# Performance work log

Measured on AMD Instinct MI355X. Metric: run time of the kernel, lower is better.

## Reference

```python
import jax, jax.numpy as jnp
import numpy as np

Q = 10        # icosahedral diamonds
M = 128       # 2**dggrid_level
L = Q * M * M # 163840 icosahedral points
KS = 9        # kernel_size / knn neighbors


def setup_inputs() -> dict:
    key = jax.random.key(0)
    k1, k2, k3, k4 = jax.random.split(key, 4)
    b, c, h, w = 1, 128, 256, 512
    x = jax.random.normal(k1, (b, c, h, w), dtype=jnp.float32)
    codeskmin = jax.random.randint(k2, (L, KS), 0, h * w, dtype=jnp.int32)
    att_w = jax.random.normal(k3, (KS, 2, KS), dtype=jnp.float32) * 0.1
    att_b = jnp.zeros((KS,), dtype=jnp.float32)
    depth_w = jax.random.normal(k4, (c, KS), dtype=jnp.float32) * 0.1
    depth_b = jnp.zeros((c,), dtype=jnp.float32)
    gamma = jnp.ones((c,), dtype=jnp.float32)
    beta = jnp.zeros((c,), dtype=jnp.float32)
    return {"x": x, "codeskmin": codeskmin, "att_w": att_w, "att_b": att_b,
            "depth_w": depth_w, "depth_b": depth_b, "gamma": gamma, "beta": beta}


def reference(x, codeskmin, att_w, att_b, depth_w, depth_b, gamma, beta):
    b, c, h, w = x.shape
    xf = x.reshape(b, c, h * w)
    # KNN gather: (b, c, L, KS)
    xe = xf[:, :, codeskmin]
    # --- SpatialAttentionModule_v1 ---
    avg = jnp.mean(xe, axis=1)           # (b, L, KS)
    mx = jnp.max(xe, axis=1)             # (b, L, KS)
    feat = jnp.stack([avg, mx], axis=1)  # (b, 2, L, KS)
    # Conv2d(2 -> KS, kernel (1,KS), no pad): reduces neighbor axis fully
    att = jnp.einsum('bilk,oik->bol', feat, att_w) + att_b[None, :, None]  # (b, KS, L)
    att = jax.nn.sigmoid(att)
    att = att.transpose(0, 2, 1)[:, None, :, :]  # (b, 1, L, KS)
    xe = att * xe + xe
    # --- depthwise conv over neighbor axis ---
    out = jnp.einsum('bclk,ck->bcl', xe, depth_w) + depth_b[None, :, None]  # (b, c, L)
    # rearrange 'b c (q h w) -> (b q) c h w'
    out = out.reshape(b, c, Q, M, M).transpose(0, 2, 1, 3, 4).reshape(b * Q, c, M, M)
    # BatchNorm (training-mode batch stats)
    mean = jnp.mean(out, axis=(0, 2, 3), keepdims=True)
    var = jnp.var(out, axis=(0, 2, 3), keepdims=True)
    out = (out - mean) * jax.lax.rsqrt(var + 1e-5)
    out = out * gamma[None, :, None, None] + beta[None, :, None, None]
    # Swish
    out = out * jax.nn.sigmoid(out)
    return out
```

## Files before the change

### kernel.cpp

```cpp
#include <hip/hip_runtime.h>
#include <hip/hip_bf16.h>

#define HW 131072
#define NCH 128
#define KS 9
#define L_TOTAL 163840
#define LPW 16

typedef float        f32x2 __attribute__((ext_vector_type(2)));
typedef float        f32x4 __attribute__((ext_vector_type(4)));

static __device__ __forceinline__ float bflo(unsigned int p) { return __uint_as_float(p << 16); }
static __device__ __forceinline__ float bfhi(unsigned int p) { return __uint_as_float(p & 0xffff0000u); }
static __device__ __forceinline__ unsigned short f2bf(float f) {
    unsigned int x = __float_as_uint(f);
    return (unsigned short)((x + 0x7fffu + ((x >> 16) & 1u)) >> 16);
}
static __device__ __forceinline__ unsigned int pack2(float a, float b) {
    return (unsigned int)f2bf(a) | ((unsigned int)f2bf(b) << 16);
}

__global__ __launch_bounds__(256) void transpose_x_kernel(
    const f32x2* __restrict__ xf,
    unsigned int* __restrict__ xT,
    float2* __restrict__ meanmaxP)
{
    __shared__ unsigned short tile[128 * 128];
    __shared__ float ps[4][128];
    __shared__ float pm[4][128];
    const int tid = threadIdx.x;
    const int lane = tid & 63;
    const int wave = tid >> 6;
    const int p0 = blockIdx.x * 128;
    const int pa = 2 * lane, pb = 2 * lane + 1;

    float s0 = 0.f, s1 = 0.f;
    float m0 = -3.4e38f, m1 = -3.4e38f;
    #pragma unroll 8
    for (int it = 0; it < 32; ++it) {
        int c = wave + (it << 2);
        f32x2 v = __builtin_nontemporal_load(&xf[(long)c * (HW / 2) + (p0 >> 1) + lane]);
        tile[pa * 128 + ((c + 2 * pa) & 127)] = f2bf(v.x);
        tile[pb * 128 + ((c + 2 * pb) & 127)] = f2bf(v.y);
        s0 += v.x; s1 += v.y;
        m0 = fmaxf(m0, v.x); m1 = fmaxf(m1, v.y);
    }
    ps[wave][pa] = s0; ps[wave][pb] = s1;
    pm[wave][pa] = m0; pm[wave][pb] = m1;
    __syncthreads();

    #pragma unroll 8
    for (int it = 0; it < 32; ++it) {
        int p = wave + (it << 2);
        int colr = (2 * lane + 2 * p) & 127;
        unsigned int d = *reinterpret_cast<const unsigned int*>(&tile[p * 128 + colr]);
        xT[(long)(p0 + p) * 64 + lane] = d;
    }
    if (tid < 128) {
        float s = ps[0][tid] + ps[1][tid] + ps[2][tid] + ps[3][tid];
        float m = fmaxf(fmaxf(pm[0][tid], pm[1][tid]), fmaxf(pm[2][tid], pm[3][tid]));
        meanmaxP[p0 + tid] = make_float2(s * 0.0078125f, m);
    }
}

__global__ __launch_bounds__(256, 6) void encoder_main_kernel(
    const unsigned int* __restrict__ xT,
    const float2* __restrict__ meanmaxP,
    const int* __restrict__ cks,
    const float* __restrict__ att_w,
    const float* __restrict__ att_b,
    const float* __restrict__ depth_w,
    const float* __restrict__ depth_b,
    unsigned int* __restrict__ ybuf,
    float* __restrict__ gsum, float* __restrict__ gsq)
{
    __shared__ __align__(16) char smem[6080];
    float* attw   = (float*)smem;
    float* attb   = (float*)(smem + 648);
    int*   lcks   = (int*)(smem + 688);
    float* mult12 = (float*)(smem + 2992);
    float* red    = (float*)smem;

    const int tid = threadIdx.x;
    const int lane = tid & 63;
    const int wave = tid >> 6;
    const int c0 = lane * 2, c1 = c0 + 1;
    const int base_l = blockIdx.x * 64;

    if (tid < 162) attw[tid] = att_w[tid];
    if (tid < KS) attb[tid] = att_b[tid];
    for (int j = tid; j < 64 * KS; j += 256) lcks[j] = cks[base_l * KS + j];

    float dw0[KS], dw1[KS];
    #pragma unroll
    for (int k = 0; k < KS; ++k) {
        dw0[k] = depth_w[c0 * KS + k];
        dw1[k] = depth_w[c1 * KS + k];
    }
    const float db0 = depth_b[c0], db1 = depth_b[c1];
    __syncthreads();

    {
        const int l_local = tid >> 2;
        const int sub = tid & 3;
        if (sub < 3) {
            float mean[KS], mx[KS];
            #pragma unroll
            for (int k = 0; k < KS; ++k) {
                float2 mm = meanmaxP[lcks[l_local * KS + k]];
                mean[k] = mm.x; mx[k] = mm.y;
            }
            #pragma unroll
            for (int oo = 0; oo < 3; ++oo) {
                int o = sub * 3 + oo;
                float logit = attb[o];
                #pragma unroll
                for (int k = 0; k < KS; ++k) {
                    logit = fmaf(mean[k], attw[o * 18 + k], logit);
                    logit = fmaf(mx[k],   attw[o * 18 + 9 + k], logit);
                }
                mult12[l_local * 12 + o] = 1.0f + 1.0f / (1.0f + __expf(-logit));
            }
        }
    }
    __syncthreads();

    float sum0 = 0.f, sum1 = 0.f, sq0 = 0.f, sq1 = 0.f;
    const int lw0 = base_l + wave * LPW;

    #pragma unroll
    for (int li = 0; li < LPW; ++li) {
        const int l = __builtin_amdgcn_readfirstlane(lw0 + li);
        const int* ckp = cks + (long)l * KS;
        int idx[KS];
        #pragma unroll
        for (int k = 0; k < KS; ++k) idx[k] = ckp[k];

        unsigned int pv[KS];
        #pragma unroll
        for (int k = 0; k < KS; ++k) {
            const unsigned int* rowp = xT + ((long)idx[k] << 6);
            pv[k] = rowp[lane];
        }

        const int ll = wave * LPW + li;
        f32x4 mA = *(const f32x4*)&mult12[ll * 12 + 0];
        f32x4 mB = *(const f32x4*)&mult12[ll * 12 + 4];
        float m8 = mult12[ll * 12 + 8];
        float mk[KS] = {mA.x, mA.y, mA.z, mA.w, mB.x, mB.y, mB.z, mB.w, m8};

        float acc0 = db0, acc1 = db1;
        #pragma unroll
        for (int k = 0; k < KS; ++k) {
            acc0 = fmaf(bflo(pv[k]) * mk[k], dw0[k], acc0);
            acc1 = fmaf(bfhi(pv[k]) * mk[k], dw1[k], acc1);
        }

        ybuf[(long)l * 64 + lane] = pack2(acc0, acc1);
        sum0 += acc0; sum1 += acc1;
        sq0 = fmaf(acc0, acc0, sq0);
        sq1 = fmaf(acc1, acc1, sq1);
    }

    __syncthreads();
    red[0 * 256 + tid] = sum0;
    red[1 * 256 + tid] = sum1;
    red[2 * 256 + tid] = sq0;
    red[3 * 256 + tid] = sq1;
    __syncthreads();

    const int grp = tid >> 6;
    const int i = tid & 63;
    float t = red[grp * 256 + i] + red[grp * 256 + 64 + i] +
              red[grp * 256 + 128 + i] + red[grp * 256 + 192 + i];
    float* dst = (grp & 2) ? gsq : gsum;
    atomicAdd(&dst[2 * i + (grp & 1)], t);
}

__global__ __launch_bounds__(256) void finalize_kernel(
    const unsigned int* __restrict__ ybuf,
    const float* __restrict__ gsum, const float* __restrict__ gsq,
    const float* __restrict__ gamma, const float* __restrict__ beta,
    float* __restrict__ out)
{
    __shared__ unsigned short tile[128 * 130];
    const int tid = threadIdx.x;
    const int lane = tid & 63;
    const int wave = tid >> 6;
    const int q = blockIdx.x >> 7;
    const int r0 = (blockIdx.x & 127) * 128;
    const int c0 = 2 * lane, c1 = c0 + 1;

    const long lbase = (long)q * 16384 + r0;
    #pragma unroll 8
    for (int it = 0; it < 32; ++it) {
        int r = wave + (it << 2);
        unsigned int u = __builtin_nontemporal_load(&ybuf[(lbase + r) * 64 + lane]);
        tile[c0 * 130 + r] = (unsigned short)(u & 0xffffu);
        tile[c1 * 130 + r] = (unsigned short)(u >> 16);
    }
    __syncthreads();

    const float invN = 1.0f / (float)L_TOTAL;
    #pragma unroll 4
    for (int it = 0; it < 32; ++it) {
        int c = wave + (it << 2);
        float m = gsum[c] * invN;
        float var = gsq[c] * invN - m * m;
        float sc = gamma[c] * rsqrtf(var + 1e-5f);
        float sh = beta[c] - m * sc;
        unsigned int d = *reinterpret_cast<const unsigned int*>(&tile[c * 130 + 2 * lane]);
        float z0 = fmaf(bflo(d), sc, sh);
        float z1 = fmaf(bfhi(d), sc, sh);
        f32x2 v;
        v.x = z0 / (1.0f + __expf(-z0));
        v.y = z1 / (1.0f + __expf(-z1));
        *(f32x2*)&out[((long)(q * NCH + c) << 14) + r0 + 2 * lane] = v;
    }
}

extern "C" void kernel_launch(void* const* d_in, const int* in_sizes, int n_in,
                              void* d_out, int out_size, void* d_ws, size_t ws_size,
                              hipStream_t stream) {
    const f32x2* x_f2  = (const f32x2*)d_in[0];
    const int* cks     = (const int*)d_in[1];
    const float* aw    = (const float*)d_in[2];
    const float* ab    = (const float*)d_in[3];
    const float* dw    = (const float*)d_in[4];
    const float* db    = (const float*)d_in[5];
    const float* gm    = (const float*)d_in[6];
    const float* bt    = (const float*)d_in[7];

    char* ws = (char*)d_ws;
    unsigned int* xT   = (unsigned int*)ws;
    float2* meanmaxP   = (float2*)(ws + 33554432);
    unsigned int* ybuf = (unsigned int*)(ws + 34603008);
    float* gsum        = (float*)(ws + 34603008 + 41943040);
    float* gsq         = gsum + NCH;

    hipMemsetAsync(gsum, 0, 2 * NCH * sizeof(float), stream);

    transpose_x_kernel<<<HW / 128, 256, 0, stream>>>(x_f2, xT, meanmaxP);
    encoder_main_kernel<<<L_TOTAL / 64, 256, 0, stream>>>(
        xT, meanmaxP, cks, aw, ab, dw, db, ybuf, gsum, gsq);
    finalize_kernel<<<1280, 256, 0, stream>>>(
        ybuf, gsum, gsq, gm, bt, (float*)d_out);
}
```

Before: 316.9 us.

## Software-pipeline neighbor gathers three rows ahead using LDS-staged indices

The main kernel now reads neighbor indices from a padded LDS copy (stride 12) instead of global memory, and keeps gathers for the next three points in flight in a rotating register buffer. The first three gathers are issued before the barrier, overlapping them with the attention computation. Stores to ybuf become nontemporal, the index load is nontemporal, and occupancy is lowered from 6 to 5 waves per SIMD to make room for the extra registers. This trades occupancy for more memory-level parallelism per wave on the random-gather loop.

```diff
diff --git a/kernel.cpp b/kernel.cpp
--- a/kernel.cpp
+++ b/kernel.cpp
@@ -63,7 +63,19 @@
     }
 }
 
-__global__ __launch_bounds__(256, 6) void encoder_main_kernel(
+#define GLD(IDX) (*(const unsigned int*)(xTc + (((unsigned)(IDX)) << 8) + (unsigned)lane4))
+#define ISSUE9(B, A0, A1, A8)            \
+    pv[B][0] = GLD((A0).x);              \
+    pv[B][1] = GLD((A0).y);              \
+    pv[B][2] = GLD((A0).z);              \
+    pv[B][3] = GLD((A0).w);              \
+    pv[B][4] = GLD((A1).x);              \
+    pv[B][5] = GLD((A1).y);              \
+    pv[B][6] = GLD((A1).z);              \
+    pv[B][7] = GLD((A1).w);              \
+    pv[B][8] = GLD(A8)
+
+__global__ __launch_bounds__(256, 5) void encoder_main_kernel(
     const unsigned int* __restrict__ xT,
     const float2* __restrict__ meanmaxP,
     const int* __restrict__ cks,
@@ -74,11 +86,11 @@
     unsigned int* __restrict__ ybuf,
     float* __restrict__ gsum, float* __restrict__ gsq)
 {
-    __shared__ __align__(16) char smem[6080];
+    __shared__ __align__(16) char smem[6832];
     float* attw   = (float*)smem;
     float* attb   = (float*)(smem + 648);
     int*   lcks   = (int*)(smem + 688);
-    float* mult12 = (float*)(smem + 2992);
+    float* mult12 = (float*)(smem + 3760);
     float* red    = (float*)smem;
 
     const int tid = threadIdx.x;
@@ -86,10 +98,15 @@
     const int wave = tid >> 6;
     const int c0 = lane * 2, c1 = c0 + 1;
     const int base_l = blockIdx.x * 64;
+    const int lane4 = lane << 2;
+    const char* xTc = (const char*)xT;
 
     if (tid < 162) attw[tid] = att_w[tid];
     if (tid < KS) attb[tid] = att_b[tid];
-    for (int j = tid; j < 64 * KS; j += 256) lcks[j] = cks[base_l * KS + j];
+    for (int j = tid; j < 64 * KS; j += 256) {
+        const int lj = j / KS;
+        lcks[lj * 12 + (j - lj * KS)] = __builtin_nontemporal_load(&cks[base_l * KS + j]);
+    }
 
     float dw0[KS], dw1[KS];
     #pragma unroll
@@ -107,7 +124,7 @@
             float mean[KS], mx[KS];
             #pragma unroll
             for (int k = 0; k < KS; ++k) {
-                float2 mm = meanmaxP[lcks[l_local * KS + k]];
+                float2 mm = meanmaxP[lcks[l_local * 12 + k]];
                 mean[k] = mm.x; mx[k] = mm.y;
             }
             #pragma unroll
@@ -123,43 +140,68 @@
             }
         }
     }
+
+    const int ll0 = wave * LPW;
+    unsigned int pv[3][KS];
+
+    #pragma unroll
+    for (int li = 0; li < 3; ++li) {
+        const int p = (ll0 + li) * 12;
+        const int4 i0 = *(const int4*)&lcks[p];
+        const int4 i1 = *(const int4*)&lcks[p + 4];
+        const int  i8 = lcks[p + 8];
+        ISSUE9(li, i0, i1, i8);
+    }
+
     __syncthreads();
 
     float sum0 = 0.f, sum1 = 0.f, sq0 = 0.f, sq1 = 0.f;
-    const int lw0 = base_l + wave * LPW;
 
     #pragma unroll
     for (int li = 0; li < LPW; ++li) {
-        const int l = __builtin_amdgcn_readfirstlane(lw0 + li);
-        const int* ckp = cks + (long)l * KS;
-        int idx[KS];
-        #pragma unroll
-        for (int k = 0; k < KS; ++k) idx[k] = ckp[k];
-
-        unsigned int pv[KS];
-        #pragma unroll
-        for (int k = 0; k < KS; ++k) {
-            const unsigned int* rowp = xT + ((long)idx[k] << 6);
-            pv[k] = rowp[lane];
+        int4 ni0 = make_int4(0, 0, 0, 0), ni1 = make_int4(0, 0, 0, 0);
+        int ni8 = 0;
+        if (li + 3 < LPW) {
+            const int p = (ll0 + li + 3) * 12;
+            ni0 = *(const int4*)&lcks[p];
+            ni1 = *(const int4*)&lcks[p + 4];
+            ni8 = lcks[p + 8];
         }
 
-        const int ll = wave * LPW + li;
-        f32x4 mA = *(const f32x4*)&mult12[ll * 12 + 0];
-        f32x4 mB = *(const f32x4*)&mult12[ll * 12 + 4];
-        float m8 = mult12[ll * 12 + 8];
-        float mk[KS] = {mA.x, mA.y, mA.z, mA.w, mB.x, mB.y, mB.z, mB.w, m8};
-
+        const int ll = ll0 + li;
+        const f32x4 mA = *(const f32x4*)&mult12[ll * 12 + 0];
+        const f32x4 mB = *(const f32x4*)&mult12[ll * 12 + 4];
+        const float m8 = mult12[ll * 12 + 8];
         float acc0 = db0, acc1 = db1;
-        #pragma unroll
-        for (int k = 0; k < KS; ++k) {
-            acc0 = fmaf(bflo(pv[k]) * mk[k], dw0[k], acc0);
-            acc1 = fmaf(bfhi(pv[k]) * mk[k], dw1[k], acc1);
-        }
-
-        ybuf[(long)l * 64 + lane] = pack2(acc0, acc1);
+
+        acc0 = fmaf(bflo(pv[li % 3][0]) * mA.x, dw0[0], acc0);
+        acc1 = fmaf(bfhi(pv[li % 3][0]) * mA.x, dw1[0], acc1);
+        acc0 = fmaf(bflo(pv[li % 3][1]) * mA.y, dw0[1], acc0);
+        acc1 = fmaf(bfhi(pv[li % 3][1]) * mA.y, dw1[1], acc1);
+        acc0 = fmaf(bflo(pv[li % 3][2]) * mA.z, dw0[2], acc0);
+        acc1 = fmaf(bfhi(pv[li % 3][2]) * mA.z, dw1[2], acc1);
+        acc0 = fmaf(bflo(pv[li % 3][3]) * mA.w, dw0[3], acc0);
+        acc1 = fmaf(bfhi(pv[li % 3][3]) * mA.w, dw1[3], acc1);
+        acc0 = fmaf(bflo(pv[li % 3][4]) * mB.x, dw0[4], acc0);
+        acc1 = fmaf(bfhi(pv[li % 3][4]) * mB.x, dw1[4], acc1);
+        acc0 = fmaf(bflo(pv[li % 3][5]) * mB.y, dw0[5], acc0);
+        acc1 = fmaf(bfhi(pv[li % 3][5]) * mB.y, dw1[5], acc1);
+        acc0 = fmaf(bflo(pv[li % 3][6]) * mB.z, dw0[6], acc0);
+        acc1 = fmaf(bfhi(pv[li % 3][6]) * mB.z, dw1[6], acc1);
+        acc0 = fmaf(bflo(pv[li % 3][7]) * mB.w, dw0[7], acc0);
+        acc1 = fmaf(bfhi(pv[li % 3][7]) * mB.w, dw1[7], acc1);
+        acc0 = fmaf(bflo(pv[li % 3][8]) * m8,   dw0[8], acc0);
+        acc1 = fmaf(bfhi(pv[li % 3][8]) * m8,   dw1[8], acc1);
+
+        __builtin_nontemporal_store(pack2(acc0, acc1),
+                                    &ybuf[(long)(base_l + ll) * 64 + lane]);
         sum0 += acc0; sum1 += acc1;
         sq0 = fmaf(acc0, acc0, sq0);
         sq1 = fmaf(acc1, acc1, sq1);
+
+        if (li + 3 < LPW) {
+            ISSUE9(li % 3, ni0, ni1, ni8);
+        }
     }
 
     __syncthreads();
```

Result: slower. 347.2 us (+9.5%).

## Split channels into 8 slabs for gather and move attention logits to separate kernel

Applied to the files above, without the earlier changes.

Lays out the bf16 transposed input and the intermediate output as 8 channel-group slabs of 16 channels each. The gather kernel now has each block handle one channel group, with 8 lanes per point, so each neighbor fetch reads 32 bytes from a smaller, more cache-resident slab instead of a 256-byte row. The attention multipliers are computed in a new kernel and staged in global memory. This adds an extra launch and an extra buffer round-trip, and it reads the neighbor indices once per channel group.

```diff
diff --git a/kernel.cpp b/kernel.cpp
--- a/kernel.cpp
+++ b/kernel.cpp
@@ -5,7 +5,8 @@
 #define NCH 128
 #define KS 9
 #define L_TOTAL 163840
-#define LPW 16
+#define NGRP 8
+#define LPB 128
 
 typedef float        f32x2 __attribute__((ext_vector_type(2)));
 typedef float        f32x4 __attribute__((ext_vector_type(4)));
@@ -54,7 +55,7 @@
         int p = wave + (it << 2);
         int colr = (2 * lane + 2 * p) & 127;
         unsigned int d = *reinterpret_cast<const unsigned int*>(&tile[p * 128 + colr]);
-        xT[(long)(p0 + p) * 64 + lane] = d;
+        xT[((long)(lane >> 3) * HW + (p0 + p)) * 8 + (lane & 7)] = d;
     }
     if (tid < 128) {
         float s = ps[0][tid] + ps[1][tid] + ps[2][tid] + ps[3][tid];
@@ -63,34 +64,80 @@
     }
 }
 
-__global__ __launch_bounds__(256, 6) void encoder_main_kernel(
-    const unsigned int* __restrict__ xT,
+__global__ __launch_bounds__(256) void mult_kernel(
     const float2* __restrict__ meanmaxP,
     const int* __restrict__ cks,
     const float* __restrict__ att_w,
     const float* __restrict__ att_b,
+    float* __restrict__ multg)
+{
+    __shared__ float attw[162];
+    __shared__ float attb[12];
+    __shared__ int lcks[64 * 12];
+    const int tid = threadIdx.x;
+    const int base_l = blockIdx.x * 64;
+
+    if (tid < 162) attw[tid] = att_w[tid];
+    if (tid < KS) attb[tid] = att_b[tid];
+    for (int j = tid; j < 64 * KS; j += 256) {
+        const int lj = j / KS;
+        lcks[lj * 12 + (j - lj * KS)] = cks[(long)base_l * KS + j];
+    }
+    __syncthreads();
+
+    const int l_local = tid >> 2;
+    const int sub = tid & 3;
+    if (sub < 3) {
+        float mean[KS], mx[KS];
+        #pragma unroll
+        for (int k = 0; k < KS; ++k) {
+            float2 mm = meanmaxP[lcks[l_local * 12 + k]];
+            mean[k] = mm.x; mx[k] = mm.y;
+        }
+        #pragma unroll
+        for (int oo = 0; oo < 3; ++oo) {
+            int o = sub * 3 + oo;
+            float logit = attb[o];
+            #pragma unroll
+            for (int k = 0; k < KS; ++k) {
+                logit = fmaf(mean[k], attw[o * 18 + k], logit);
+                logit = fmaf(mx[k],   attw[o * 18 + 9 + k], logit);
+            }
+            multg[(long)(base_l + l_local) * 12 + o] = 1.0f + 1.0f / (1.0f + __expf(-logit));
+        }
+    }
+}
+
+__global__ __launch_bounds__(256, 6) void gather_kernel(
+    const unsigned int* __restrict__ xT,
+    const int* __restrict__ cks,
+    const float* __restrict__ multg,
     const float* __restrict__ depth_w,
     const float* __restrict__ depth_b,
     unsigned int* __restrict__ ybuf,
     float* __restrict__ gsum, float* __restrict__ gsq)
 {
-    __shared__ __align__(16) char smem[6080];
-    float* attw   = (float*)smem;
-    float* attb   = (float*)(smem + 648);
-    int*   lcks   = (int*)(smem + 688);
-    float* mult12 = (float*)(smem + 2992);
-    float* red    = (float*)smem;
-
-    const int tid = threadIdx.x;
+    __shared__ __align__(16) char smem[12288];
+    int*   lcks = (int*)smem;
+    float* mult = (float*)(smem + 6144);
+    float* red  = (float*)smem;
+
+    const int tid  = threadIdx.x;
     const int lane = tid & 63;
     const int wave = tid >> 6;
-    const int c0 = lane * 2, c1 = c0 + 1;
-    const int base_l = blockIdx.x * 64;
-
-    if (tid < 162) attw[tid] = att_w[tid];
-    if (tid < KS) attb[tid] = att_b[tid];
-    for (int j = tid; j < 64 * KS; j += 256) lcks[j] = cks[base_l * KS + j];
-
+    const int g      = blockIdx.x & 7;
+    const int base_l = (blockIdx.x >> 3) * LPB;
+    const int d    = lane & 7;
+    const int lsub = lane >> 3;
+
+    for (int j = tid; j < LPB * KS; j += 256) {
+        const int lj = j / KS;
+        lcks[lj * 12 + (j - lj * KS)] = __builtin_nontemporal_load(&cks[(long)base_l * KS + j]);
+    }
+    for (int j = tid; j < LPB * 12; j += 256)
+        mult[j] = __builtin_nontemporal_load(&multg[(long)base_l * 12 + j]);
+
+    const int c0 = g * 16 + 2 * d, c1 = c0 + 1;
     float dw0[KS], dw1[KS];
     #pragma unroll
     for (int k = 0; k < KS; ++k) {
@@ -98,65 +145,56 @@
         dw1[k] = depth_w[c1 * KS + k];
     }
     const float db0 = depth_b[c0], db1 = depth_b[c1];
-    __syncthreads();
-
-    {
-        const int l_local = tid >> 2;
-        const int sub = tid & 3;
-        if (sub < 3) {
-            float mean[KS], mx[KS];
-            #pragma unroll
-            for (int k = 0; k < KS; ++k) {
-                float2 mm = meanmaxP[lcks[l_local * KS + k]];
-                mean[k] = mm.x; mx[k] = mm.y;
-            }
-            #pragma unroll
-            for (int oo = 0; oo < 3; ++oo) {
-                int o = sub * 3 + oo;
-                float logit = attb[o];
-                #pragma unroll
-                for (int k = 0; k < KS; ++k) {
-                    logit = fmaf(mean[k], attw[o * 18 + k], logit);
-                    logit = fmaf(mx[k],   attw[o * 18 + 9 + k], logit);
-                }
-                mult12[l_local * 12 + o] = 1.0f + 1.0f / (1.0f + __expf(-logit));
-            }
-        }
-    }
+
+    const unsigned int* slab  = xT   + (long)g * HW * 8;
+    unsigned int*       yslab = ybuf + (long)g * L_TOTAL * 8;
     __syncthreads();
 
     float sum0 = 0.f, sum1 = 0.f, sq0 = 0.f, sq1 = 0.f;
-    const int lw0 = base_l + wave * LPW;
+    const int l0 = wave * (LPB / 4);
 
     #pragma unroll
-    for (int li = 0; li < LPW; ++li) {
-        const int l = __builtin_amdgcn_readfirstlane(lw0 + li);
-        const int* ckp = cks + (long)l * KS;
-        int idx[KS];
-        #pragma unroll
-        for (int k = 0; k < KS; ++k) idx[k] = ckp[k];
-
-        unsigned int pv[KS];
-        #pragma unroll
-        for (int k = 0; k < KS; ++k) {
-            const unsigned int* rowp = xT + ((long)idx[k] << 6);
-            pv[k] = rowp[lane];
-        }
-
-        const int ll = wave * LPW + li;
-        f32x4 mA = *(const f32x4*)&mult12[ll * 12 + 0];
-        f32x4 mB = *(const f32x4*)&mult12[ll * 12 + 4];
-        float m8 = mult12[ll * 12 + 8];
-        float mk[KS] = {mA.x, mA.y, mA.z, mA.w, mB.x, mB.y, mB.z, mB.w, m8};
+    for (int oct = 0; oct < LPB / 32; ++oct) {
+        const int l = l0 + oct * 8 + lsub;
+        const int4 i0 = *(const int4*)&lcks[l * 12];
+        const int4 i1 = *(const int4*)&lcks[l * 12 + 4];
+        const int  i8 = lcks[l * 12 + 8];
+
+        unsigned int pv0 = slab[(long)(unsigned)i0.x * 8 + d];
+        unsigned int pv1 = slab[(long)(unsigned)i0.y * 8 + d];
+        unsigned int pv2 = slab[(long)(unsigned)i0.z * 8 + d];
+        unsigned int pv3 = slab[(long)(unsigned)i0.w * 8 + d];
+        unsigned int pv4 = slab[(long)(unsigned)i1.x * 8 + d];
+        unsigned int pv5 = slab[(long)(unsigned)i1.y * 8 + d];
+        unsigned int pv6 = slab[(long)(unsigned)i1.z * 8 + d];
+        unsigned int pv7 = slab[(long)(unsigned)i1.w * 8 + d];
+        unsigned int pv8 = slab[(long)(unsigned)i8   * 8 + d];
+
+        const f32x4 mA = *(const f32x4*)&mult[l * 12];
+        const f32x4 mB = *(const f32x4*)&mult[l * 12 + 4];
+        const float m8 = mult[l * 12 + 8];
 
         float acc0 = db0, acc1 = db1;
-        #pragma unroll
-        for (int k = 0; k < KS; ++k) {
-            acc0 = fmaf(bflo(pv[k]) * mk[k], dw0[k], acc0);
-            acc1 = fmaf(bfhi(pv[k]) * mk[k], dw1[k], acc1);
-        }
-
-        ybuf[(long)l * 64 + lane] = pack2(acc0, acc1);
+        acc0 = fmaf(bflo(pv0) * mA.x, dw0[0], acc0);
+        acc1 = fmaf(bfhi(pv0) * mA.x, dw1[0], acc1);
+        acc0 = fmaf(bflo(pv1) * mA.y, dw0[1], acc0);
+        acc1 = fmaf(bfhi(pv1) * mA.y, dw1[1], acc1);
+        acc0 = fmaf(bflo(pv2) * mA.z, dw0[2], acc0);
+        acc1 = fmaf(bfhi(pv2) * mA.z, dw1[2], acc1);
+        acc0 = fmaf(bflo(pv3) * mA.w, dw0[3], acc0);
+        acc1 = fmaf(bfhi(pv3) * mA.w, dw1[3], acc1);
+        acc0 = fmaf(bflo(pv4) * mB.x, dw0[4], acc0);
+        acc1 = fmaf(bfhi(pv4) * mB.x, dw1[4], acc1);
+        acc0 = fmaf(bflo(pv5) * mB.y, dw0[5], acc0);
+        acc1 = fmaf(bfhi(pv5) * mB.y, dw1[5], acc1);
+        acc0 = fmaf(bflo(pv6) * mB.z, dw0[6], acc0);
+        acc1 = fmaf(bfhi(pv6) * mB.z, dw1[6], acc1);
+        acc0 = fmaf(bflo(pv7) * mB.w, dw0[7], acc0);
+        acc1 = fmaf(bfhi(pv7) * mB.w, dw1[7], acc1);
+        acc0 = fmaf(bflo(pv8) * m8,   dw0[8], acc0);
+        acc1 = fmaf(bfhi(pv8) * m8,   dw1[8], acc1);
+
+        yslab[(long)(base_l + l) * 8 + d] = pack2(acc0, acc1);
         sum0 += acc0; sum1 += acc1;
         sq0 = fmaf(acc0, acc0, sq0);
         sq1 = fmaf(acc1, acc1, sq1);
@@ -173,8 +211,18 @@
     const int i = tid & 63;
     float t = red[grp * 256 + i] + red[grp * 256 + 64 + i] +
               red[grp * 256 + 128 + i] + red[grp * 256 + 192 + i];
-    float* dst = (grp & 2) ? gsq : gsum;
-    atomicAdd(&dst[2 * i + (grp & 1)], t);
+    float* red2 = red + 1024;
+    red2[grp * 64 + i] = t;
+    __syncthreads();
+
+    if (tid < 32) {
+        const int q = tid >> 3, dd = tid & 7;
+        float s = 0.f;
+        #pragma unroll
+        for (int j = 0; j < 8; ++j) s += red2[q * 64 + j * 8 + dd];
+        float* dst = (q & 2) ? gsq : gsum;
+        atomicAdd(&dst[g * 16 + 2 * dd + (q & 1)], s);
+    }
 }
 
 __global__ __launch_bounds__(256) void finalize_kernel(
@@ -189,13 +237,15 @@
     const int wave = tid >> 6;
     const int q = blockIdx.x >> 7;
     const int r0 = (blockIdx.x & 127) * 128;
-    const int c0 = 2 * lane, c1 = c0 + 1;
+    const int gg = lane >> 3, dd = lane & 7;
+    const int c0 = gg * 16 + 2 * dd, c1 = c0 + 1;
 
     const long lbase = (long)q * 16384 + r0;
     #pragma unroll 8
     for (int it = 0; it < 32; ++it) {
         int r = wave + (it << 2);
-        unsigned int u = __builtin_nontemporal_load(&ybuf[(lbase + r) * 64 + lane]);
+        unsigned int u = __builtin_nontemporal_load(
+            &ybuf[((long)gg * L_TOTAL + lbase + r) * 8 + dd]);
         tile[c0 * 130 + r] = (unsigned short)(u & 0xffffu);
         tile[c1 * 130 + r] = (unsigned short)(u >> 16);
     }
@@ -235,14 +285,16 @@
     unsigned int* xT   = (unsigned int*)ws;
     float2* meanmaxP   = (float2*)(ws + 33554432);
     unsigned int* ybuf = (unsigned int*)(ws + 34603008);
-    float* gsum        = (float*)(ws + 34603008 + 41943040);
+    float* multg       = (float*)(ws + 76546048);
+    float* gsum        = (float*)(ws + 84410368);
     float* gsq         = gsum + NCH;
 
     hipMemsetAsync(gsum, 0, 2 * NCH * sizeof(float), stream);
 
     transpose_x_kernel<<<HW / 128, 256, 0, stream>>>(x_f2, xT, meanmaxP);
-    encoder_main_kernel<<<L_TOTAL / 64, 256, 0, stream>>>(
-        xT, meanmaxP, cks, aw, ab, dw, db, ybuf, gsum, gsq);
+    mult_kernel<<<L_TOTAL / 64, 256, 0, stream>>>(meanmaxP, cks, aw, ab, multg);
+    gather_kernel<<<(L_TOTAL / LPB) * NGRP, 256, 0, stream>>>(
+        xT, cks, multg, dw, db, ybuf, gsum, gsq);
     finalize_kernel<<<1280, 256, 0, stream>>>(
         ybuf, gsum, gsq, gm, bt, (float*)d_out);
 }
```

Result: faster. 303.4 us (-4.3%).

## Split channel-grouped gather into separate kernel with packed index/attention records

Applied to the files above, without the earlier changes.

Re-lays xT and ybuf into 8 channel-group slabs of 16 channels each, so each gather block touches a 4 MB slab that can stay L2-resident instead of scattering across the full 32 MB table. The attention multiplier is computed in a separate kernel and packed with the neighbor index into one 32-bit record (17-bit index, 15-bit quantized sigmoid). The gather kernel then reads these records and does 8-byte channel loads per lane, with shuffle-based stats reduction. This adds a kernel launch and quantizes the attention weight to 15 bits, which introduces small approximation error.

```diff
diff --git a/kernel.cpp b/kernel.cpp
--- a/kernel.cpp
+++ b/kernel.cpp
@@ -5,10 +5,13 @@
 #define NCH 128
 #define KS 9
 #define L_TOTAL 163840
-#define LPW 16
+#define NGRP 8
+#define LPB 128
 
 typedef float        f32x2 __attribute__((ext_vector_type(2)));
 typedef float        f32x4 __attribute__((ext_vector_type(4)));
+typedef unsigned int u32x2 __attribute__((ext_vector_type(2)));
+typedef unsigned int u32x4 __attribute__((ext_vector_type(4)));
 
 static __device__ __forceinline__ float bflo(unsigned int p) { return __uint_as_float(p << 16); }
 static __device__ __forceinline__ float bfhi(unsigned int p) { return __uint_as_float(p & 0xffff0000u); }
@@ -54,7 +57,7 @@
         int p = wave + (it << 2);
         int colr = (2 * lane + 2 * p) & 127;
         unsigned int d = *reinterpret_cast<const unsigned int*>(&tile[p * 128 + colr]);
-        xT[(long)(p0 + p) * 64 + lane] = d;
+        xT[((long)(lane >> 3) * HW + (p0 + p)) * 8 + (lane & 7)] = d;
     }
     if (tid < 128) {
         float s = ps[0][tid] + ps[1][tid] + ps[2][tid] + ps[3][tid];
@@ -63,118 +66,160 @@
     }
 }
 
-__global__ __launch_bounds__(256, 6) void encoder_main_kernel(
-    const unsigned int* __restrict__ xT,
+__global__ __launch_bounds__(256) void mult_kernel(
     const float2* __restrict__ meanmaxP,
     const int* __restrict__ cks,
     const float* __restrict__ att_w,
     const float* __restrict__ att_b,
+    unsigned int* __restrict__ rec)
+{
+    __shared__ float attw[162];
+    __shared__ float attb[12];
+    __shared__ int lcks[64 * 12];
+    const int tid = threadIdx.x;
+    const int base_l = blockIdx.x * 64;
+
+    if (tid < 162) attw[tid] = att_w[tid];
+    if (tid < KS) attb[tid] = att_b[tid];
+    for (int j = tid; j < 64 * KS; j += 256) {
+        const int lj = j / KS;
+        lcks[lj * 12 + (j - lj * KS)] = cks[(long)base_l * KS + j];
+    }
+    __syncthreads();
+
+    const int l_local = tid >> 2;
+    const int sub = tid & 3;
+    if (sub < 3) {
+        float mean[KS], mx[KS];
+        #pragma unroll
+        for (int k = 0; k < KS; ++k) {
+            float2 mm = meanmaxP[lcks[l_local * 12 + k]];
+            mean[k] = mm.x; mx[k] = mm.y;
+        }
+        #pragma unroll
+        for (int oo = 0; oo < 3; ++oo) {
+            int o = sub * 3 + oo;
+            float logit = attb[o];
+            #pragma unroll
+            for (int k = 0; k < KS; ++k) {
+                logit = fmaf(mean[k], attw[o * 18 + k], logit);
+                logit = fmaf(mx[k],   attw[o * 18 + 9 + k], logit);
+            }
+            float sig = 1.0f / (1.0f + __expf(-logit));
+            unsigned int u = (unsigned int)(sig * 32768.0f + 0.5f);
+            if (u > 32767u) u = 32767u;
+            rec[(long)(base_l + l_local) * 12 + o] =
+                (unsigned int)lcks[l_local * 12 + o] | (u << 17);
+        }
+    }
+}
+
+__global__ __launch_bounds__(256, 4) void gather_kernel(
+    const unsigned int* __restrict__ xT,
+    const unsigned int* __restrict__ rec,
     const float* __restrict__ depth_w,
     const float* __restrict__ depth_b,
     unsigned int* __restrict__ ybuf,
     float* __restrict__ gsum, float* __restrict__ gsq)
 {
-    __shared__ __align__(16) char smem[6080];
-    float* attw   = (float*)smem;
-    float* attb   = (float*)(smem + 648);
-    int*   lcks   = (int*)(smem + 688);
-    float* mult12 = (float*)(smem + 2992);
-    float* red    = (float*)smem;
-
-    const int tid = threadIdx.x;
+    __shared__ float dwl[KS][16];
+    __shared__ float dbl[16];
+    __shared__ float redx[4][4][8];
+
+    const int tid  = threadIdx.x;
     const int lane = tid & 63;
     const int wave = tid >> 6;
-    const int c0 = lane * 2, c1 = c0 + 1;
-    const int base_l = blockIdx.x * 64;
-
-    if (tid < 162) attw[tid] = att_w[tid];
-    if (tid < KS) attb[tid] = att_b[tid];
-    for (int j = tid; j < 64 * KS; j += 256) lcks[j] = cks[base_l * KS + j];
-
-    float dw0[KS], dw1[KS];
+    const int g      = blockIdx.x & 7;
+    const int base_l = (blockIdx.x >> 3) * LPB;
+    const int qt = lane & 3;
+    const int lq = lane >> 2;
+
+    if (tid < 144) {
+        int k = tid >> 4, ch = tid & 15;
+        dwl[k][ch] = depth_w[(g * 16 + ch) * KS + k];
+    }
+    if (tid < 16) dbl[tid] = depth_b[g * 16 + tid];
+    __syncthreads();
+
+    f32x2 dw[KS][2];
     #pragma unroll
     for (int k = 0; k < KS; ++k) {
-        dw0[k] = depth_w[c0 * KS + k];
-        dw1[k] = depth_w[c1 * KS + k];
-    }
-    const float db0 = depth_b[c0], db1 = depth_b[c1];
-    __syncthreads();
-
+        f32x4 t = *(const f32x4*)&dwl[k][qt * 4];
+        dw[k][0].x = t.x; dw[k][0].y = t.y;
+        dw[k][1].x = t.z; dw[k][1].y = t.w;
+    }
+    f32x2 db01, db23;
     {
-        const int l_local = tid >> 2;
-        const int sub = tid & 3;
-        if (sub < 3) {
-            float mean[KS], mx[KS];
-            #pragma unroll
-            for (int k = 0; k < KS; ++k) {
-                float2 mm = meanmaxP[lcks[l_local * KS + k]];
-                mean[k] = mm.x; mx[k] = mm.y;
-            }
-            #pragma unroll
-            for (int oo = 0; oo < 3; ++oo) {
-                int o = sub * 3 + oo;
-                float logit = attb[o];
-                #pragma unroll
-                for (int k = 0; k < KS; ++k) {
-                    logit = fmaf(mean[k], attw[o * 18 + k], logit);
-                    logit = fmaf(mx[k],   attw[o * 18 + 9 + k], logit);
-                }
-                mult12[l_local * 12 + o] = 1.0f + 1.0f / (1.0f + __expf(-logit));
-            }
+        f32x4 t = *(const f32x4*)&dbl[qt * 4];
+        db01.x = t.x; db01.y = t.y; db23.x = t.z; db23.y = t.w;
+    }
+
+    const unsigned int* slab  = xT   + ((size_t)g << 20);
+    unsigned int*       yslab = ybuf + (size_t)g * (L_TOTAL * 8);
+
+    f32x2 sum01 = {0.f, 0.f}, sum23 = {0.f, 0.f};
+    f32x2 sq01  = {0.f, 0.f}, sq23  = {0.f, 0.f};
+
+    #pragma unroll
+    for (int b = 0; b < 2; ++b) {
+        const int lloc = wave * 32 + b * 16 + lq;
+        const unsigned int* rp = rec + (size_t)(base_l + lloc) * 12;
+        const u32x4 r0 = __builtin_nontemporal_load((const u32x4*)rp);
+        const u32x4 r1 = __builtin_nontemporal_load((const u32x4*)(rp + 4));
+        const unsigned int r8 = __builtin_nontemporal_load(rp + 8);
+        const unsigned int rr[KS] = {r0.x, r0.y, r0.z, r0.w,
+                                     r1.x, r1.y, r1.z, r1.w, r8};
+
+        u32x2 pv[KS];
+        #pragma unroll
+        for (int k = 0; k < KS; ++k)
+            pv[k] = *(const u32x2*)(slab + ((rr[k] & 0x1FFFFu) << 3) + (qt << 1));
+
+        f32x2 acc01 = db01, acc23 = db23;
+        #pragma unroll
+        for (int k = 0; k < KS; ++k) {
+            const float mk = fmaf((float)(rr[k] >> 17), 3.0517578125e-5f, 1.0f);
+            f32x2 mk2; mk2.x = mk; mk2.y = mk;
+            f32x2 xa; xa.x = bflo(pv[k].x); xa.y = bfhi(pv[k].x);
+            f32x2 xb; xb.x = bflo(pv[k].y); xb.y = bfhi(pv[k].y);
+            acc01 = __builtin_elementwise_fma(xa * mk2, dw[k][0], acc01);
+            acc23 = __builtin_elementwise_fma(xb * mk2, dw[k][1], acc23);
         }
-    }
-    __syncthreads();
-
-    float sum0 = 0.f, sum1 = 0.f, sq0 = 0.f, sq1 = 0.f;
-    const int lw0 = base_l + wave * LPW;
+
+        u32x2 o;
+        o.x = pack2(acc01.x, acc01.y);
+        o.y = pack2(acc23.x, acc23.y);
+        *(u32x2*)(yslab + (size_t)(base_l + lloc) * 8 + (qt << 1)) = o;
+
+        sum01 += acc01; sum23 += acc23;
+        sq01 = __builtin_elementwise_fma(acc01, acc01, sq01);
+        sq23 = __builtin_elementwise_fma(acc23, acc23, sq23);
+    }
 
     #pragma unroll
-    for (int li = 0; li < LPW; ++li) {
-        const int l = __builtin_amdgcn_readfirstlane(lw0 + li);
-        const int* ckp = cks + (long)l * KS;
-        int idx[KS];
-        #pragma unroll
-        for (int k = 0; k < KS; ++k) idx[k] = ckp[k];
-
-        unsigned int pv[KS];
-        #pragma unroll
-        for (int k = 0; k < KS; ++k) {
-            const unsigned int* rowp = xT + ((long)idx[k] << 6);
-            pv[k] = rowp[lane];
-        }
-
-        const int ll = wave * LPW + li;
-        f32x4 mA = *(const f32x4*)&mult12[ll * 12 + 0];
-        f32x4 mB = *(const f32x4*)&mult12[ll * 12 + 4];
-        float m8 = mult12[ll * 12 + 8];
-        float mk[KS] = {mA.x, mA.y, mA.z, mA.w, mB.x, mB.y, mB.z, mB.w, m8};
-
-        float acc0 = db0, acc1 = db1;
-        #pragma unroll
-        for (int k = 0; k < KS; ++k) {
-            acc0 = fmaf(bflo(pv[k]) * mk[k], dw0[k], acc0);
-            acc1 = fmaf(bfhi(pv[k]) * mk[k], dw1[k], acc1);
-        }
-
-        ybuf[(long)l * 64 + lane] = pack2(acc0, acc1);
-        sum0 += acc0; sum1 += acc1;
-        sq0 = fmaf(acc0, acc0, sq0);
-        sq1 = fmaf(acc1, acc1, sq1);
-    }
-
-    __syncthreads();
-    red[0 * 256 + tid] = sum0;
-    red[1 * 256 + tid] = sum1;
-    red[2 * 256 + tid] = sq0;
-    red[3 * 256 + tid] = sq1;
-    __syncthreads();
-
-    const int grp = tid >> 6;
-    const int i = tid & 63;
-    float t = red[grp * 256 + i] + red[grp * 256 + 64 + i] +
-              red[grp * 256 + 128 + i] + red[grp * 256 + 192 + i];
-    float* dst = (grp & 2) ? gsq : gsum;
-    atomicAdd(&dst[2 * i + (grp & 1)], t);
+    for (int s = 4; s <= 32; s <<= 1) {
+        sum01.x += __shfl_xor(sum01.x, s);
+        sum01.y += __shfl_xor(sum01.y, s);
+        sum23.x += __shfl_xor(sum23.x, s);
+        sum23.y += __shfl_xor(sum23.y, s);
+        sq01.x  += __shfl_xor(sq01.x,  s);
+        sq01.y  += __shfl_xor(sq01.y,  s);
+        sq23.x  += __shfl_xor(sq23.x,  s);
+        sq23.y  += __shfl_xor(sq23.y,  s);
+    }
+    if (lane < 4) {
+        float* rw = &redx[wave][lane][0];
+        rw[0] = sum01.x; rw[1] = sum01.y; rw[2] = sum23.x; rw[3] = sum23.y;
+        rw[4] = sq01.x;  rw[5] = sq01.y;  rw[6] = sq23.x;  rw[7] = sq23.y;
+    }
+    __syncthreads();
+    if (tid < 32) {
+        const int q = tid >> 2, qq = tid & 3;
+        float s = redx[0][qq][q] + redx[1][qq][q] + redx[2][qq][q] + redx[3][qq][q];
+        const int ch = g * 16 + qq * 4 + (q & 3);
+        float* dst = (q >= 4) ? gsq : gsum;
+        atomicAdd(&dst[ch], s);
+    }
 }
 
 __global__ __launch_bounds__(256) void finalize_kernel(
@@ -189,13 +234,15 @@
     const int wave = tid >> 6;
     const int q = blockIdx.x >> 7;
     const int r0 = (blockIdx.x & 127) * 128;
-    const int c0 = 2 * lane, c1 = c0 + 1;
+    const int gg = lane >> 3, dd = lane & 7;
+    const int c0 = gg * 16 + 2 * dd, c1 = c0 + 1;
 
     const long lbase = (long)q * 16384 + r0;
     #pragma unroll 8
     for (int it = 0; it < 32; ++it) {
         int r = wave + (it << 2);
-        unsigned int u = __builtin_nontemporal_load(&ybuf[(lbase + r) * 64 + lane]);
+        unsigned int u = __builtin_nontemporal_load(
+            &ybuf[((long)gg * L_TOTAL + lbase + r) * 8 + dd]);
         tile[c0 * 130 + r] = (unsigned short)(u & 0xffffu);
         tile[c1 * 130 + r] = (unsigned short)(u >> 16);
     }
@@ -235,14 +282,16 @@
     unsigned int* xT   = (unsigned int*)ws;
     float2* meanmaxP   = (float2*)(ws + 33554432);
     unsigned int* ybuf = (unsigned int*)(ws + 34603008);
-    float* gsum        = (float*)(ws + 34603008 + 41943040);
+    unsigned int* rec  = (unsigned int*)(ws + 76546048);
+    float* gsum        = (float*)(ws + 84410368);
     float* gsq         = gsum + NCH;
 
     hipMemsetAsync(gsum, 0, 2 * NCH * sizeof(float), stream);
 
     transpose_x_kernel<<<HW / 128, 256, 0, stream>>>(x_f2, xT, meanmaxP);
-    encoder_main_kernel<<<L_TOTAL / 64, 256, 0, stream>>>(
-        xT, meanmaxP, cks, aw, ab, dw, db, ybuf, gsum, gsq);
+    mult_kernel<<<L_TOTAL / 64, 256, 0, stream>>>(meanmaxP, cks, aw, ab, rec);
+    gather_kernel<<<(L_TOTAL / LPB) * NGRP, 256, 0, stream>>>(
+        xT, rec, dw, db, ybuf, gsum, gsq);
     finalize_kernel<<<1280, 256, 0, stream>>>(
         ybuf, gsum, gsq, gm, bt, (float*)d_out);
 }
```

Result: faster. 300.3 us (-5.2%).
